# Performance work log

Hardware: AMD Instinct MI355X
Metric: run time of the kernel (lower is better)

The kernel has to match this reference:

```python
import jax, jax.numpy as jnp
import numpy as np

GROUPS = 32
EPS = 1e-5
NUM_HEADS = 8


def group_norm(x, gamma, beta):
    B, C, H, W = x.shape
    xg = x.reshape(B, GROUPS, C // GROUPS, H, W)
    mean = xg.mean(axis=(2, 3, 4), keepdims=True)
    var = xg.var(axis=(2, 3, 4), keepdims=True)
    xg = (xg - mean) * jax.lax.rsqrt(var + EPS)
    x = xg.reshape(B, C, H, W)
    return x * gamma[None, :, None, None] + beta[None, :, None, None]


def setup_inputs() -> dict:
    key = jax.random.key(0)
    k1, k2, k3 = jax.random.split(key, 3)
    C = 512
    x = jax.random.normal(k1, (16, C, 32, 32), dtype=jnp.float32)
    gn_gamma = jnp.ones((C,), dtype=jnp.float32)
    gn_beta = jnp.zeros((C,), dtype=jnp.float32)
    w_qkv = jax.random.normal(k2, (3 * C, C), dtype=jnp.float32) * 0.02
    b_qkv = jnp.zeros((3 * C,), dtype=jnp.float32)
    w_proj = jax.random.normal(k3, (C, C), dtype=jnp.float32) * 0.02
    b_proj = jnp.zeros((C,), dtype=jnp.float32)
    return {"x": x, "gn_gamma": gn_gamma, "gn_beta": gn_beta,
            "w_qkv": w_qkv, "b_qkv": b_qkv, "w_proj": w_proj, "b_proj": b_proj}


def reference(x, gn_gamma, gn_beta, w_qkv, b_qkv, w_proj, b_proj):
    B, C, H, W = x.shape
    nh = NUM_HEADS
    hd = C // nh
    h = group_norm(x, gn_gamma, gn_beta)
    # 1x1 conv == channel matmul: [B,3C,H,W]
    qkv = jnp.einsum('bchw,oc->bohw', h, w_qkv) + b_qkv[None, :, None, None]
    qkv = qkv.reshape(B, 3, nh, hd, H * W)
    q, k, v = qkv[:, 0], qkv[:, 1], qkv[:, 2]  # [B, nh, hd, HW]
    scale = hd ** -0.5
    # attn[b,n,i,j] = sum_d q[b,n,d,i] * k[b,n,d,j]
    attn = jax.nn.softmax(jnp.einsum('bndi,bndj->bnij', q, k) * scale, axis=-1)
    # h[b,n,d,i] = sum_j v[b,n,d,j] * attn[b,n,i,j]
    h = jnp.einsum('bndj,bnij->bndi', v, attn).reshape(B, C, H, W)
    out = jnp.einsum('bchw,oc->bohw', h, w_proj) + b_proj[None, :, None, None]
    return x + out
```

## Files before the change

kernel.cpp:

```cpp
#include <hip/hip_runtime.h>

typedef __bf16 bf16;
typedef __bf16 bf16x2 __attribute__((ext_vector_type(2)));
typedef __bf16 bf16x4 __attribute__((ext_vector_type(4)));
typedef __bf16 bf16x8 __attribute__((ext_vector_type(8)));
typedef float  f32x4  __attribute__((ext_vector_type(4)));
typedef float  f32x16 __attribute__((ext_vector_type(16)));
typedef unsigned int u32x4 __attribute__((ext_vector_type(4)));

#define MFMA32(a,b,c) __builtin_amdgcn_mfma_f32_32x32x16_bf16((a),(b),(c),0,0,0)

#if __has_builtin(__builtin_amdgcn_exp2f)
#define EXP2(x) __builtin_amdgcn_exp2f(x)
#else
#define EXP2(x) exp2f(x)
#endif

__device__ __forceinline__ void gll16(const void* g, void* l) {
  __builtin_amdgcn_global_load_lds((const __attribute__((address_space(1))) unsigned int*)g,
                                   (__attribute__((address_space(3))) unsigned int*)l, 16, 0, 0);
}

__device__ __forceinline__ unsigned pk2(float a, float b) {
  bf16x2 t = { (bf16)a, (bf16)b };
  return __builtin_bit_cast(unsigned, t);
}

__device__ __forceinline__ void pl32swap(unsigned &x, unsigned &y) {
  asm("v_permlane32_swap_b32 %0, %1" : "+v"(x), "+v"(y));
}

static constexpr int Cc = 512;
static constexpr int Ss = 1024;
#define QSCALE 0.18033688011112042f

__global__ __launch_bounds__(256) void k_wconv(const float* __restrict__ wq, const float* __restrict__ wp,
                                               bf16* __restrict__ wqb, bf16* __restrict__ wpb) {
  const int i = blockIdx.x * 256 + threadIdx.x;
  if (i * 4 < 786432) {
    float4 v = ((const float4*)wq)[i];
    bf16x4 o = { (bf16)v.x, (bf16)v.y, (bf16)v.z, (bf16)v.w };
    ((bf16x4*)wqb)[i] = o;
  } else {
    const int j = i - 786432 / 4;
    float4 v = ((const float4*)wp)[j];
    bf16x4 o = { (bf16)v.x, (bf16)v.y, (bf16)v.z, (bf16)v.w };
    ((bf16x4*)wpb)[j] = o;
  }
}

__global__ __launch_bounds__(256, 2) void k_gnorm(const float* __restrict__ x,
                                                  const float* __restrict__ gamma,
                                                  const float* __restrict__ beta,
                                                  bf16* __restrict__ ht) {
  const int g = blockIdx.x;
  const int b = blockIdx.y;
  const float* base = x + ((size_t)b * Cc + g * 16) * Ss;
  const int tid = threadIdx.x;

  f32x4 xr[16];
  float s = 0.f, sq = 0.f;
  #pragma unroll
  for (int k = 0; k < 16; ++k) {
    xr[k] = ((const f32x4*)base)[k * 256 + tid];
    s  += xr[k][0] + xr[k][1] + xr[k][2] + xr[k][3];
    sq += xr[k][0] * xr[k][0] + xr[k][1] * xr[k][1] + xr[k][2] * xr[k][2] + xr[k][3] * xr[k][3];
  }
  #pragma unroll
  for (int m = 1; m < 64; m <<= 1) { s += __shfl_xor(s, m); sq += __shfl_xor(sq, m); }
  __shared__ float red[8];
  if ((tid & 63) == 0) { red[tid >> 6] = s; red[4 + (tid >> 6)] = sq; }
  __syncthreads();
  const float stot = red[0] + red[1] + red[2] + red[3];
  const float sqt  = red[4] + red[5] + red[6] + red[7];
  const float mean = stot * (1.f / 16384.f);
  const float var  = sqt * (1.f / 16384.f) - mean * mean;
  const float rstd = rsqrtf(var + 1e-5f);

  float ga[16], bb[16];
  #pragma unroll
  for (int k = 0; k < 16; ++k) {
    ga[k] = gamma[g * 16 + k] * rstd;
    bb[k] = beta[g * 16 + k] - mean * ga[k];
  }

  bf16* dst0 = ht + ((size_t)b * Ss + tid * 4) * Cc + g * 16;
  #pragma unroll
  for (int j = 0; j < 4; ++j) {
    bf16x8 o0, o1;
    #pragma unroll
    for (int k = 0; k < 8; ++k)  o0[k] = (bf16)(xr[k][j] * ga[k] + bb[k]);
    #pragma unroll
    for (int k = 0; k < 8; ++k)  o1[k] = (bf16)(xr[8 + k][j] * ga[8 + k] + bb[8 + k]);
    bf16* d = dst0 + (size_t)j * Cc;
    *(bf16x8*)d = o0;
    *(bf16x8*)(d + 8) = o1;
  }
}

template<int MODE>
__global__ __launch_bounds__(256, 2) void k_gemm(const bf16* __restrict__ Aw,
                                                 const bf16* __restrict__ Bt,
                                                 const float* __restrict__ bias,
                                                 bf16* __restrict__ qo, bf16* __restrict__ ko,
                                                 bf16* __restrict__ vo,
                                                 const float* __restrict__ xres,
                                                 float* __restrict__ out) {
  const int nt = blockIdx.x, mt = blockIdx.y, b = blockIdx.z;
  const int M0 = mt * 128, N0 = nt * 128;
  __shared__ __align__(16) char lA[2][16384];
  __shared__ __align__(16) char lB[2][16384];
  const int tid = threadIdx.x;
  const int l = tid & 63, w = tid >> 6;
  const int wm = w >> 1, wn = w & 1;
  const int l31 = l & 31, h = l >> 5;
  const bf16* Bb = Bt + (size_t)b * Ss * Cc;

  const int r8 = tid >> 3, c8 = tid & 7;
  const int csw = (c8 ^ (r8 & 7)) * 16;
  const char* asrc = (const char*)Aw + (size_t)(M0 + r8) * 1024 + csw;
  const char* bsrc = (const char*)Bb + (size_t)(N0 + r8) * 1024 + csw;
  const int dstoff = tid * 16;

  f32x16 acc[2][2];
  #pragma unroll
  for (int i = 0; i < 2; ++i)
    #pragma unroll
    for (int j = 0; j < 2; ++j)
      #pragma unroll
      for (int r = 0; r < 16; ++r) acc[i][j][r] = 0.f;

  const int sw7 = l31 & 7;

  #pragma unroll
  for (int p = 0; p < 4; ++p)
    gll16(asrc + (size_t)p * 32768, (char*)lA[0] + dstoff + p * 4096);
  #pragma unroll
  for (int p = 0; p < 4; ++p)
    gll16(bsrc + (size_t)p * 32768, (char*)lB[0] + dstoff + p * 4096);

  #pragma unroll
  for (int kt = 0; kt < 8; ++kt) {
    const int cur = kt & 1;
    if (kt < 7) {
      #pragma unroll
      for (int p = 0; p < 4; ++p)
        gll16(asrc + (size_t)p * 32768 + (kt + 1) * 128, (char*)lA[cur ^ 1] + dstoff + p * 4096);
      #pragma unroll
      for (int p = 0; p < 4; ++p)
        gll16(bsrc + (size_t)p * 32768 + (kt + 1) * 128, (char*)lB[cur ^ 1] + dstoff + p * 4096);
      asm volatile("s_waitcnt vmcnt(8)" ::: "memory");
    } else {
      asm volatile("s_waitcnt vmcnt(0)" ::: "memory");
    }
    __builtin_amdgcn_s_barrier();
    __builtin_amdgcn_sched_barrier(0);

    __builtin_amdgcn_s_setprio(1);
    #pragma unroll
    for (int kb = 0; kb < 4; ++kb) {
      const int cA0 = ((kb * 2 + h) ^ sw7) * 16;
      const int rA0 = (wm * 2 + 0) * 32 + l31, rA1 = (wm * 2 + 1) * 32 + l31;
      const int rB0 = (wn * 2 + 0) * 32 + l31, rB1 = (wn * 2 + 1) * 32 + l31;
      bf16x8 a0 = *(const bf16x8*)((const char*)lA[cur] + rA0 * 128 + cA0);
      bf16x8 a1 = *(const bf16x8*)((const char*)lA[cur] + rA1 * 128 + cA0);
      bf16x8 b0 = *(const bf16x8*)((const char*)lB[cur] + rB0 * 128 + cA0);
      bf16x8 b1 = *(const bf16x8*)((const char*)lB[cur] + rB1 * 128 + cA0);
      acc[0][0] = MFMA32(a0, b0, acc[0][0]);
      acc[0][1] = MFMA32(a0, b1, acc[0][1]);
      acc[1][0] = MFMA32(a1, b0, acc[1][0]);
      acc[1][1] = MFMA32(a1, b1, acc[1][1]);
    }
    __builtin_amdgcn_s_setprio(0);
    if (kt < 7) {
      asm volatile("s_waitcnt lgkmcnt(0)" ::: "memory");
      __builtin_amdgcn_s_barrier();
    }
  }

  #pragma unroll
  for (int m = 0; m < 2; ++m) {
    const int ofr = M0 + wm * 64 + m * 32;
    #pragma unroll
    for (int n = 0; n < 2; ++n) {
      const int sI = N0 + wn * 64 + n * 32 + l31;
      #pragma unroll
      for (int Qi = 0; Qi < 4; ++Qi) {
        const int rb = Qi * 8 + h * 4;
        float v[4], bi[4];
        #pragma unroll
        for (int r = 0; r < 4; ++r) {
          v[r] = acc[m][n][Qi * 4 + r];
          bi[r] = bias[ofr + rb + r];
        }
        if (MODE == 0) {
          const int which = ofr >> 9;
          const int nh = (ofr >> 6) & 7;
          const int dbase = (ofr & 63) + rb;
          const size_t bh = (size_t)b * 8 + nh;
          if (which == 2) {
            #pragma unroll
            for (int r = 0; r < 4; ++r)
              vo[(bh * 64 + dbase + r) * 1024 + sI] = (bf16)(v[r] + bi[r]);
          } else {
            const float qs = which ? 1.f : QSCALE;
            bf16x4 pk = { (bf16)((v[0] + bi[0]) * qs), (bf16)((v[1] + bi[1]) * qs),
                          (bf16)((v[2] + bi[2]) * qs), (bf16)((v[3] + bi[3]) * qs) };
            bf16* dst = (which ? ko : qo) + (bh * 1024 + sI) * 64 + dbase;
            *(bf16x4*)dst = pk;
          }
        } else {
          #pragma unroll
          for (int r = 0; r < 4; ++r) {
            const size_t idx = ((size_t)b * 512 + ofr + rb + r) * 1024 + sI;
            out[idx] = xres[idx] + bi[r] + v[r];
          }
        }
      }
    }
  }
}

__global__ __launch_bounds__(512, 2) void k_attn(const bf16* __restrict__ qT,
                                                 const bf16* __restrict__ kT,
                                                 const bf16* __restrict__ vv,
                                                 bf16* __restrict__ ao) {
  const int it = blockIdx.x, nh = blockIdx.y, b = blockIdx.z;
  const size_t bh = (size_t)b * 8 + nh;
  const char* kh = (const char*)(kT + bh * 65536);
  const char* vh = (const char*)(vv + bh * 65536);
  __shared__ __align__(16) char smem[32768];
  const int tid = threadIdx.x;
  const int w = tid >> 6, l = tid & 63;
  const int l31 = l & 31, h = l >> 5;

  const bf16* qrow = qT + bh * 65536 + (size_t)(it * 512 + w * 64 + l31) * 64;
  bf16x8 qf[2][4];
  #pragma unroll
  for (int qb = 0; qb < 2; ++qb)
    #pragma unroll
    for (int kq = 0; kq < 4; ++kq)
      qf[qb][kq] = *(const bf16x8*)(qrow + qb * 2048 + kq * 16 + h * 8);

  const int ct = tid >> 6, c3 = ct & 3, c2 = ct >> 2;
  const char* ksrc = kh + (size_t)(c2 * 32 + l31) * 128 + c3 * 32 + h * 16;
  const char* vsrc = vh + (size_t)(c2 * 32 + l31) * 2048 + c3 * 32 + h * 16;
  char* lkdst = smem + tid * 16;
  char* lvdst = smem + 16384 + tid * 16;

  gll16(ksrc, lkdst);
  gll16(vsrc, lvdst);

  f32x16 oacc[2][2];
  #pragma unroll
  for (int qb = 0; qb < 2; ++qb)
    #pragma unroll
    for (int dt = 0; dt < 2; ++dt)
      #pragma unroll
      for (int r = 0; r < 16; ++r) oacc[qb][dt][r] = 0.f;
  float lacc[2][2] = {{0.f, 0.f}, {0.f, 0.f}};

  int cur = 0;
  for (int t = 0; t < 16; ++t) {
    if (t < 15) {
      gll16(ksrc + (size_t)(t + 1) * 8192, lkdst + (cur ^ 1) * 8192);
      gll16(vsrc + (size_t)(t + 1) * 128,  lvdst + (cur ^ 1) * 8192);
      asm volatile("s_waitcnt vmcnt(2)" ::: "memory");
    } else {
      asm volatile("s_waitcnt vmcnt(0)" ::: "memory");
    }
    __builtin_amdgcn_s_barrier();
    __builtin_amdgcn_sched_barrier(0);

    const char* lkc = smem + cur * 8192;
    const char* lvc = smem + 16384 + cur * 8192;

    bf16x8 pb[2][4];
    #pragma unroll
    for (int jt = 0; jt < 2; ++jt) {
      f32x16 sf[2];
      #pragma unroll
      for (int r = 0; r < 16; ++r) { sf[0][r] = 0.f; sf[1][r] = 0.f; }
      __builtin_amdgcn_s_setprio(1);
      #pragma unroll
      for (int kq = 0; kq < 4; ++kq) {
        bf16x8 a = *(const bf16x8*)(lkc + (jt * 4 + kq) * 1024 + l * 16);
        sf[0] = MFMA32(a, qf[0][kq], sf[0]);
        sf[1] = MFMA32(a, qf[1][kq], sf[1]);
      }
      __builtin_amdgcn_s_setprio(0);
      #pragma unroll
      for (int qb = 0; qb < 2; ++qb) {
        unsigned pw[4][2];
        #pragma unroll
        for (int Qi = 0; Qi < 4; ++Qi) {
          const float p0 = EXP2(sf[qb][Qi * 4 + 0]);
          const float p1 = EXP2(sf[qb][Qi * 4 + 1]);
          const float p2 = EXP2(sf[qb][Qi * 4 + 2]);
          const float p3 = EXP2(sf[qb][Qi * 4 + 3]);
          lacc[qb][0] += p0 + p1; lacc[qb][1] += p2 + p3;
          pw[Qi][0] = pk2(p0, p1);
          pw[Qi][1] = pk2(p2, p3);
        }
        #pragma unroll
        for (int sq = 0; sq < 2; ++sq) {
          unsigned x0 = pw[2 * sq][0], y0 = pw[2 * sq + 1][0];
          unsigned x1 = pw[2 * sq][1], y1 = pw[2 * sq + 1][1];
          pl32swap(x0, y0);
          pl32swap(x1, y1);
          u32x4 wv = { x0, x1, y0, y1 };
          pb[qb][jt * 2 + sq] = __builtin_bit_cast(bf16x8, wv);
        }
      }
    }

    __builtin_amdgcn_s_setprio(1);
    #pragma unroll
    for (int dt = 0; dt < 2; ++dt) {
      #pragma unroll
      for (int s = 0; s < 4; ++s) {
        bf16x8 av = *(const bf16x8*)(lvc + (dt * 4 + s) * 1024 + l * 16);
        oacc[0][dt] = MFMA32(av, pb[0][s], oacc[0][dt]);
        oacc[1][dt] = MFMA32(av, pb[1][s], oacc[1][dt]);
      }
    }
    __builtin_amdgcn_s_setprio(0);
    if (t < 15) {
      asm volatile("s_waitcnt lgkmcnt(0)" ::: "memory");
      __builtin_amdgcn_s_barrier();
    }
    cur ^= 1;
  }

  #pragma unroll
  for (int qb = 0; qb < 2; ++qb) {
    float ls = lacc[qb][0] + lacc[qb][1];
    ls += __shfl_xor(ls, 32);
    const float rinv = 1.f / ls;
    bf16* aor = ao + ((size_t)b * 1024 + it * 512 + w * 64 + qb * 32 + l31) * 512 + nh * 64;
    #pragma unroll
    for (int dt = 0; dt < 2; ++dt) {
      #pragma unroll
      for (int Qi = 0; Qi < 4; ++Qi) {
        bf16x4 o = { (bf16)(oacc[qb][dt][Qi * 4 + 0] * rinv), (bf16)(oacc[qb][dt][Qi * 4 + 1] * rinv),
                     (bf16)(oacc[qb][dt][Qi * 4 + 2] * rinv), (bf16)(oacc[qb][dt][Qi * 4 + 3] * rinv) };
        *(bf16x4*)(aor + dt * 32 + Qi * 8 + h * 4) = o;
      }
    }
  }
}

extern "C" void kernel_launch(void* const* d_in, const int* in_sizes, int n_in,
                              void* d_out, int out_size, void* d_ws, size_t ws_size,
                              hipStream_t stream) {
  (void)in_sizes; (void)n_in; (void)out_size; (void)ws_size;
  const float* x   = (const float*)d_in[0];
  const float* gam = (const float*)d_in[1];
  const float* bet = (const float*)d_in[2];
  const float* wq  = (const float*)d_in[3];
  const float* bq  = (const float*)d_in[4];
  const float* wp  = (const float*)d_in[5];
  const float* bp  = (const float*)d_in[6];
  float* out = (float*)d_out;

  bf16* ws  = (bf16*)d_ws;
  bf16* ht  = ws;
  bf16* qT  = ws + 8388608;
  bf16* kT  = ws + 16777216;
  bf16* vv  = ws + 25165824;
  bf16* wqb = ws + 33554432;
  bf16* wpb = ws + 34340864;

  k_wconv<<<1024, 256, 0, stream>>>(wq, wp, wqb, wpb);
  k_gnorm<<<dim3(32, 16), 256, 0, stream>>>(x, gam, bet, ht);
  k_gemm<0><<<dim3(8, 12, 16), 256, 0, stream>>>(wqb, ht, bq, qT, kT, vv, nullptr, nullptr);
  k_attn<<<dim3(2, 8, 16), 512, 0, stream>>>(qT, kT, vv, ht);
  k_gemm<1><<<dim3(8, 4, 16), 256, 0, stream>>>(wpb, ht, bp, nullptr, nullptr, nullptr, x, out);
}
```

Measured before the change: 126.1 us.

## Triple-buffer K/V tiles in attention and halve block size to 256 threads

```diff
diff --git a/kernel.cpp b/kernel.cpp
--- a/kernel.cpp
+++ b/kernel.cpp
@@ -221,7 +221,7 @@
   }
 }
 
-__global__ __launch_bounds__(512, 2) void k_attn(const bf16* __restrict__ qT,
+__global__ __launch_bounds__(256, 2) void k_attn(const bf16* __restrict__ qT,
                                                  const bf16* __restrict__ kT,
                                                  const bf16* __restrict__ vv,
                                                  bf16* __restrict__ ao) {
@@ -229,12 +229,12 @@
   const size_t bh = (size_t)b * 8 + nh;
   const char* kh = (const char*)(kT + bh * 65536);
   const char* vh = (const char*)(vv + bh * 65536);
-  __shared__ __align__(16) char smem[32768];
+  __shared__ __align__(16) char smem[49152];
   const int tid = threadIdx.x;
   const int w = tid >> 6, l = tid & 63;
   const int l31 = l & 31, h = l >> 5;
 
-  const bf16* qrow = qT + bh * 65536 + (size_t)(it * 512 + w * 64 + l31) * 64;
+  const bf16* qrow = qT + bh * 65536 + (size_t)(it * 256 + w * 64 + l31) * 64;
   bf16x8 qf[2][4];
   #pragma unroll
   for (int qb = 0; qb < 2; ++qb)
@@ -242,14 +242,20 @@
     for (int kq = 0; kq < 4; ++kq)
       qf[qb][kq] = *(const bf16x8*)(qrow + qb * 2048 + kq * 16 + h * 8);
 
-  const int ct = tid >> 6, c3 = ct & 3, c2 = ct >> 2;
-  const char* ksrc = kh + (size_t)(c2 * 32 + l31) * 128 + c3 * 32 + h * 16;
-  const char* vsrc = vh + (size_t)(c2 * 32 + l31) * 2048 + c3 * 32 + h * 16;
-  char* lkdst = smem + tid * 16;
-  char* lvdst = smem + 16384 + tid * 16;
-
-  gll16(ksrc, lkdst);
-  gll16(vsrc, lvdst);
+  const int c3 = tid >> 6;
+  const int l31s = l & 31, hs = l >> 5;
+  const char* ksrc = kh + (size_t)l31s * 128 + c3 * 32 + hs * 16;
+  const char* vsrc = vh + (size_t)l31s * 2048 + c3 * 32 + hs * 16;
+  char* lkd = smem + tid * 16;
+  char* lvd = smem + 24576 + tid * 16;
+
+  #pragma unroll
+  for (int t0 = 0; t0 < 2; ++t0) {
+    gll16(ksrc + (size_t)t0 * 8192,         lkd + t0 * 8192);
+    gll16(ksrc + (size_t)t0 * 8192 + 4096,  lkd + t0 * 8192 + 4096);
+    gll16(vsrc + (size_t)t0 * 128,          lvd + t0 * 8192);
+    gll16(vsrc + (size_t)t0 * 128 + 65536,  lvd + t0 * 8192 + 4096);
+  }
 
   f32x16 oacc[2][2];
   #pragma unroll
@@ -260,20 +266,22 @@
       for (int r = 0; r < 16; ++r) oacc[qb][dt][r] = 0.f;
   float lacc[2][2] = {{0.f, 0.f}, {0.f, 0.f}};
 
-  int cur = 0;
+  int slot = 0;
   for (int t = 0; t < 16; ++t) {
-    if (t < 15) {
-      gll16(ksrc + (size_t)(t + 1) * 8192, lkdst + (cur ^ 1) * 8192);
-      gll16(vsrc + (size_t)(t + 1) * 128,  lvdst + (cur ^ 1) * 8192);
-      asm volatile("s_waitcnt vmcnt(2)" ::: "memory");
-    } else {
-      asm volatile("s_waitcnt vmcnt(0)" ::: "memory");
-    }
+    if (t < 15) asm volatile("s_waitcnt vmcnt(4)" ::: "memory");
+    else        asm volatile("s_waitcnt vmcnt(0)" ::: "memory");
     __builtin_amdgcn_s_barrier();
     __builtin_amdgcn_sched_barrier(0);
-
-    const char* lkc = smem + cur * 8192;
-    const char* lvc = smem + 16384 + cur * 8192;
+    if (t <= 13) {
+      const int sn = (slot == 0) ? 2 : slot - 1;
+      gll16(ksrc + (size_t)(t + 2) * 8192,        lkd + sn * 8192);
+      gll16(ksrc + (size_t)(t + 2) * 8192 + 4096, lkd + sn * 8192 + 4096);
+      gll16(vsrc + (size_t)(t + 2) * 128,         lvd + sn * 8192);
+      gll16(vsrc + (size_t)(t + 2) * 128 + 65536, lvd + sn * 8192 + 4096);
+    }
+
+    const char* lkc = smem + slot * 8192;
+    const char* lvc = smem + 24576 + slot * 8192;
 
     bf16x8 pb[2][4];
     #pragma unroll
@@ -325,11 +333,7 @@
       }
     }
     __builtin_amdgcn_s_setprio(0);
-    if (t < 15) {
-      asm volatile("s_waitcnt lgkmcnt(0)" ::: "memory");
-      __builtin_amdgcn_s_barrier();
-    }
-    cur ^= 1;
+    slot = (slot == 2) ? 0 : slot + 1;
   }
 
   #pragma unroll
@@ -337,7 +341,7 @@
     float ls = lacc[qb][0] + lacc[qb][1];
     ls += __shfl_xor(ls, 32);
     const float rinv = 1.f / ls;
-    bf16* aor = ao + ((size_t)b * 1024 + it * 512 + w * 64 + qb * 32 + l31) * 512 + nh * 64;
+    bf16* aor = ao + ((size_t)b * 1024 + it * 256 + w * 64 + qb * 32 + l31) * 512 + nh * 64;
     #pragma unroll
     for (int dt = 0; dt < 2; ++dt) {
       #pragma unroll
@@ -374,6 +378,6 @@
   k_wconv<<<1024, 256, 0, stream>>>(wq, wp, wqb, wpb);
   k_gnorm<<<dim3(32, 16), 256, 0, stream>>>(x, gam, bet, ht);
   k_gemm<0><<<dim3(8, 12, 16), 256, 0, stream>>>(wqb, ht, bq, qT, kT, vv, nullptr, nullptr);
-  k_attn<<<dim3(2, 8, 16), 512, 0, stream>>>(qT, kT, vv, ht);
+  k_attn<<<dim3(4, 8, 16), 256, 0, stream>>>(qT, kT, vv, ht);
   k_gemm<1><<<dim3(8, 4, 16), 256, 0, stream>>>(wpb, ht, bp, nullptr, nullptr, nullptr, x, out);
 }
```

Result: no change. 126.0 us (-0.1%).
